# Kernel tuning notes

Measured on AMD Instinct MI355X. Metric: run time of the kernel, lower is better.

The kernel has to match this reference:

```python
import jax, jax.numpy as jnp
import numpy as np

TOKENS = 4096
IN_FEATURES = 4096
OUT_FEATURES = 4096
NNZ = 512  # nonzeros per output row, multiple of 4 so vectorize-pad is a no-op


def setup_inputs() -> dict:
    key = jax.random.key(0)
    k1, k2, k3, k4 = jax.random.split(key, 4)
    x = jax.random.normal(k1, (TOKENS, IN_FEATURES), dtype=jnp.float32)
    w = jax.random.normal(k2, (OUT_FEATURES, NNZ), dtype=jnp.float32)
    # sorted per-row column indices, mimicking nonzero() order of a pruned row
    mask = jnp.sort(
        jax.random.randint(k3, (OUT_FEATURES, NNZ), 0, IN_FEATURES, dtype=jnp.int32),
        axis=-1,
    )
    b = jax.random.normal(k4, (OUT_FEATURES,), dtype=jnp.float32)
    return {"input": x, "condensed_weight": w, "input_mask": mask, "bias": b}


def reference(input, condensed_weight, input_mask, bias):
    # y[t, o] = sum_k input[t, input_mask[o, k]] * condensed_weight[o, k] + bias[o]
    # Scatter condensed rows back to a dense [O, In] weight, then GEMM.
    # .add handles duplicate / padded (index 0, weight 0) entries exactly like
    # the gather-multiply-reduce formulation.
    O, K = condensed_weight.shape
    In = input.shape[-1]
    rows = jnp.arange(O, dtype=input_mask.dtype)[:, None]  # [O, 1]
    W = jnp.zeros((O, In), dtype=condensed_weight.dtype).at[rows, input_mask].add(condensed_weight)
    return input @ W.T + bias
```

## Files before the change

### kernel.cpp

```cpp
#include <hip/hip_runtime.h>
#include <hip/hip_bf16.h>
#include <stdint.h>

#define TOKENS 4096
#define IN_F   4096
#define OUT_F  4096
#define NNZ    512

using floatx4 = __attribute__((ext_vector_type(4))) float;
using bf16x8  = __attribute__((ext_vector_type(8))) __bf16;

__device__ __forceinline__ unsigned short f2bf(float f) {
    unsigned int u = __float_as_uint(f);
    u += 0x7FFFu + ((u >> 16) & 1u);
    return (unsigned short)(u >> 16);
}

__global__ __launch_bounds__(256) void prep_fused(
        const float* __restrict__ x,
        const float* __restrict__ w,
        const int*   __restrict__ mask,
        unsigned short* __restrict__ Xb,
        unsigned short* __restrict__ Wb) {
    __shared__ unsigned short row[IN_F];
    const int b = blockIdx.x;
    const int t = threadIdx.x;

    if (b < OUT_F) {
        uint4* rv = (uint4*)row;
        rv[t]       = make_uint4(0u, 0u, 0u, 0u);
        rv[t + 256] = make_uint4(0u, 0u, 0u, 0u);
        __syncthreads();

        const int base = b * NNZ;
#pragma unroll
        for (int e = 0; e < 2; ++e) {
            const int k = t + e * 256;
            const int idx = mask[base + k];
            if (k == 0 || mask[base + k - 1] != idx) {
                float s = w[base + k];
                int j = k + 1;
                while (j < NNZ && mask[base + j] == idx) { s += w[base + j]; ++j; }
                row[idx] = f2bf(s);
            }
        }
        __syncthreads();

        uint4* out = (uint4*)(Wb + (size_t)b * IN_F);
        out[t]       = rv[t];
        out[t + 256] = rv[t + 256];
    } else {
        const int i = (b - OUT_F) * 256 + t;
        const float4* xv = (const float4*)x;
        float4 a = xv[2 * i];
        float4 c = xv[2 * i + 1];
        uint4 o;
        o.x = (unsigned)f2bf(a.x) | ((unsigned)f2bf(a.y) << 16);
        o.y = (unsigned)f2bf(a.z) | ((unsigned)f2bf(a.w) << 16);
        o.z = (unsigned)f2bf(c.x) | ((unsigned)f2bf(c.y) << 16);
        o.w = (unsigned)f2bf(c.z) | ((unsigned)f2bf(c.w) << 16);
        ((uint4*)Xb)[i] = o;
    }
}


#define GLL16(src, dst) \
    __builtin_amdgcn_global_load_lds((__attribute__((address_space(1))) void*)(src), \
                                     (__attribute__((address_space(3))) void*)(dst), 16, 0, 0)

__global__ __launch_bounds__(512, 2) void gemm_bt_bias(
        const unsigned short* __restrict__ A,
        const unsigned short* __restrict__ B,
        const float* __restrict__ bias,
        float* __restrict__ C) {
    __shared__ unsigned short As[2][16384];
    __shared__ unsigned short Bs[2][16384];

    const int tid  = threadIdx.x;
    const int wave = tid >> 6;
    const int lane = tid & 63;
    const int lq   = lane >> 4;
    const int lm   = lane & 15;
    const int lm7  = lm & 7;
    const int wm2  = wave >> 2;
    const int wn4  = wave & 3;

    const int bid = blockIdx.x;
    const int swz = (bid & 7) * 32 + (bid >> 3);
    const int m0  = (swz >> 4) << 8;
    const int n0  = (swz & 15) << 8;

    const int r   = tid >> 3;
    const int cse = ((tid & 7) ^ (r & 7)) * 8;
    const int oAX0 = (m0 + r)       * IN_F + cse;
    const int oAX1 = (m0 + 128 + r) * IN_F + cse;
    const int oAY0 = (m0 +  64 + r) * IN_F + cse;
    const int oAY1 = (m0 + 192 + r) * IN_F + cse;
    const int bc_  = (r >> 5) * 64 + (r & 31);
    const int oBU0 = (n0 + bc_)        * IN_F + cse;
    const int oBU1 = (n0 + 128 + bc_)  * IN_F + cse;
    const int oBV0 = (n0 +  32 + bc_)  * IN_F + cse;
    const int oBV1 = (n0 + 160 + bc_)  * IN_F + cse;
    const int wofs = wave * 512;

#define STAGE_AX(bb, kk) { GLL16(A + oAX0 + (kk), &As[bb][        wofs]); \
                           GLL16(A + oAX1 + (kk), &As[bb][ 4096 + wofs]); }
#define STAGE_AY(bb, kk) { GLL16(A + oAY0 + (kk), &As[bb][ 8192 + wofs]); \
                           GLL16(A + oAY1 + (kk), &As[bb][12288 + wofs]); }
#define STAGE_BU(bb, kk) { GLL16(B + oBU0 + (kk), &Bs[bb][        wofs]); \
                           GLL16(B + oBU1 + (kk), &Bs[bb][ 4096 + wofs]); }
#define STAGE_BV(bb, kk) { GLL16(B + oBV0 + (kk), &Bs[bb][ 8192 + wofs]); \
                           GLL16(B + oBV1 + (kk), &Bs[bb][12288 + wofs]); }

    const int ck0 = (lq ^ lm7) * 8;
    const int ck1 = ck0 ^ 32;
    const int aX  = (wm2 * 64 + lm) * 64;
    const int aY  = aX + 8192;
    const int bU  = (wn4 * 32 + lm) * 64;
    const int bV  = bU + 8192;

    floatx4 acc[8][4] = {};
    bf16x8 af[4][2], bu[2][2], bv[2][2];

    STAGE_AX(0, 0); STAGE_BU(0, 0); STAGE_BV(0, 0); STAGE_AY(0, 0);
    STAGE_AX(1, 64); STAGE_BU(1, 64); STAGE_BV(1, 64);
    asm volatile("s_waitcnt vmcnt(6)" ::: "memory");
    __builtin_amdgcn_s_barrier();

#define TILE_STEP(T, BB)                                                          \
    {                                                                             \
        const unsigned short* sA = As[BB];                                        \
        const unsigned short* sB = Bs[BB];                                        \
        const int kk1 = ((T) + 1 < 64 ? (T) + 1 : 63) * 64;                       \
        const int kk2 = ((T) + 2 < 64 ? (T) + 2 : 63) * 64;                       \
                                                      \
        _Pragma("unroll")                                                         \
        for (int mi = 0; mi < 4; ++mi) {                                          \
            af[mi][0] = *(const bf16x8*)(sA + aX + mi * 1024 + ck0);              \
            af[mi][1] = *(const bf16x8*)(sA + aX + mi * 1024 + ck1);              \
        }                                                                         \
        _Pragma("unroll")                                                         \
        for (int ni = 0; ni < 2; ++ni) {                                          \
            bu[ni][0] = *(const bf16x8*)(sB + bU + ni * 1024 + ck0);              \
            bu[ni][1] = *(const bf16x8*)(sB + bU + ni * 1024 + ck1);              \
        }                                                                         \
        STAGE_AY((BB) ^ 1, kk1);                                                  \
        asm volatile("s_waitcnt lgkmcnt(8)" ::: "memory");                        \
        __builtin_amdgcn_s_barrier();                                             \
        asm volatile("s_waitcnt lgkmcnt(0)" ::: "memory");                        \
        __builtin_amdgcn_s_setprio(1);                                            \
        _Pragma("unroll")                                                         \
        for (int mi = 0; mi < 4; ++mi)                                            \
            _Pragma("unroll")                                                     \
            for (int ni = 0; ni < 2; ++ni) {                                      \
                acc[mi][ni] = __builtin_amdgcn_mfma_f32_16x16x32_bf16(            \
                    af[mi][0], bu[ni][0], acc[mi][ni], 0, 0, 0);                  \
                acc[mi][ni] = __builtin_amdgcn_mfma_f32_16x16x32_bf16(            \
                    af[mi][1], bu[ni][1], acc[mi][ni], 0, 0, 0);                  \
            }                                                                     \
        __builtin_amdgcn_s_setprio(0);                                            \
        __builtin_amdgcn_s_barrier();                                             \
                                                      \
        _Pragma("unroll")                                                         \
        for (int ni = 0; ni < 2; ++ni) {                                          \
            bv[ni][0] = *(const bf16x8*)(sB + bV + ni * 1024 + ck0);              \
            bv[ni][1] = *(const bf16x8*)(sB + bV + ni * 1024 + ck1);              \
        }                                                                         \
        STAGE_AX((BB), kk2);                                                      \
        __builtin_amdgcn_s_barrier();                                             \
        asm volatile("s_waitcnt lgkmcnt(0)" ::: "memory");                        \
        __builtin_amdgcn_s_setprio(1);                                            \
        _Pragma("unroll")                                                         \
        for (int mi = 0; mi < 4; ++mi)                                            \
            _Pragma("unroll")                                                     \
            for (int ni = 0; ni < 2; ++ni) {                                      \
                acc[mi][2 + ni] = __builtin_amdgcn_mfma_f32_16x16x32_bf16(        \
                    af[mi][0], bv[ni][0], acc[mi][2 + ni], 0, 0, 0);              \
                acc[mi][2 + ni] = __builtin_amdgcn_mfma_f32_16x16x32_bf16(        \
                    af[mi][1], bv[ni][1], acc[mi][2 + ni], 0, 0, 0);              \
            }                                                                     \
        __builtin_amdgcn_s_setprio(0);                                            \
        __builtin_amdgcn_s_barrier();                                             \
                                                      \
        _Pragma("unroll")                                                         \
        for (int mi = 0; mi < 4; ++mi) {                                          \
            af[mi][0] = *(const bf16x8*)(sA + aY + mi * 1024 + ck0);              \
            af[mi][1] = *(const bf16x8*)(sA + aY + mi * 1024 + ck1);              \
        }                                                                         \
        STAGE_BU((BB), kk2);                                                      \
        __builtin_amdgcn_s_barrier();                                             \
        asm volatile("s_waitcnt lgkmcnt(0)" ::: "memory");                        \
        __builtin_amdgcn_s_setprio(1);                                            \
        _Pragma("unroll")                                                         \
        for (int mi = 0; mi < 4; ++mi)                                            \
            _Pragma("unroll")                                                     \
            for (int ni = 0; ni < 2; ++ni) {                                      \
                acc[4 + mi][2 + ni] = __builtin_amdgcn_mfma_f32_16x16x32_bf16(    \
                    af[mi][0], bv[ni][0], acc[4 + mi][2 + ni], 0, 0, 0);          \
                acc[4 + mi][2 + ni] = __builtin_amdgcn_mfma_f32_16x16x32_bf16(    \
                    af[mi][1], bv[ni][1], acc[4 + mi][2 + ni], 0, 0, 0);          \
            }                                                                     \
        __builtin_amdgcn_s_setprio(0);                                            \
        __builtin_amdgcn_s_barrier();                                             \
                                \
        STAGE_BV((BB), kk2);                                                      \
        __builtin_amdgcn_s_barrier();                                             \
        __builtin_amdgcn_s_setprio(1);                                            \
        _Pragma("unroll")                                                         \
        for (int mi = 0; mi < 4; ++mi)                                            \
            _Pragma("unroll")                                                     \
            for (int ni = 0; ni < 2; ++ni) {                                      \
                acc[4 + mi][ni] = __builtin_amdgcn_mfma_f32_16x16x32_bf16(        \
                    af[mi][0], bu[ni][0], acc[4 + mi][ni], 0, 0, 0);              \
                acc[4 + mi][ni] = __builtin_amdgcn_mfma_f32_16x16x32_bf16(        \
                    af[mi][1], bu[ni][1], acc[4 + mi][ni], 0, 0, 0);              \
            }                                                                     \
        __builtin_amdgcn_s_setprio(0);                                            \
        asm volatile("s_waitcnt vmcnt(6)" ::: "memory");                          \
        __builtin_amdgcn_s_barrier();                                             \
    }

    for (int tt = 0; tt < 32; ++tt) {
        TILE_STEP(2 * tt,     0);
        TILE_STEP(2 * tt + 1, 1);
    }

#pragma unroll
    for (int ni = 0; ni < 4; ++ni) {
        const int n = n0 + wn4 * 64 + ni * 16 + lm;
        const float bb = bias[n];
#pragma unroll
        for (int mi = 0; mi < 8; ++mi) {
            const int mb = m0 + wm2 * 128 + mi * 16 + lq * 4;
#pragma unroll
            for (int rr = 0; rr < 4; ++rr) {
                C[(size_t)(mb + rr) * OUT_F + n] = acc[mi][ni][rr] + bb;
            }
        }
    }
}

extern "C" void kernel_launch(void* const* d_in, const int* in_sizes, int n_in,
                              void* d_out, int out_size, void* d_ws, size_t ws_size,
                              hipStream_t stream) {
    const float* x    = (const float*)d_in[0];
    const float* w    = (const float*)d_in[1];
    const int*   mask = (const int*)d_in[2];
    const float* bias = (const float*)d_in[3];
    float* out = (float*)d_out;

    unsigned short* Xb = (unsigned short*)d_ws;
    unsigned short* Wb = Xb + (size_t)TOKENS * IN_F;

    prep_fused<<<OUT_F + 8192, 256, 0, stream>>>(x, w, mask, Xb, Wb);
    gemm_bt_bias<<<dim3(256), dim3(512), 0, stream>>>(Xb, Wb, bias, out);
}
```

Before: 253.8 us.

## Restructure prep kernel to wave-per-row densify and multi-element cast, nontemporal output stores

The weight densify step now assigns one wavefront per output row, with four rows per block, and uses vectorized int4/float4 loads plus a per-lane run-merge. This removes block-wide barriers and the per-element scan over neighbouring mask entries. The input cast blocks each process four chunks, so the grid shrinks from 12288 to 3072 blocks. The GEMM epilogue writes C with nontemporal stores to avoid polluting cache. Fewer blocks could reduce the latency hiding available in the prep kernel.

```diff
diff --git a/kernel.cpp b/kernel.cpp
--- a/kernel.cpp
+++ b/kernel.cpp
@@ -22,44 +22,65 @@
         const int*   __restrict__ mask,
         unsigned short* __restrict__ Xb,
         unsigned short* __restrict__ Wb) {
-    __shared__ unsigned short row[IN_F];
+    __shared__ unsigned short rows[4][IN_F];
     const int b = blockIdx.x;
     const int t = threadIdx.x;
 
-    if (b < OUT_F) {
+    if (b < 1024) {
+        const int wave = t >> 6;
+        const int lane = t & 63;
+        const int rrow = b * 4 + wave;
+        unsigned short* row = rows[wave];
         uint4* rv = (uint4*)row;
-        rv[t]       = make_uint4(0u, 0u, 0u, 0u);
-        rv[t + 256] = make_uint4(0u, 0u, 0u, 0u);
-        __syncthreads();
-
-        const int base = b * NNZ;
-#pragma unroll
-        for (int e = 0; e < 2; ++e) {
-            const int k = t + e * 256;
-            const int idx = mask[base + k];
-            if (k == 0 || mask[base + k - 1] != idx) {
-                float s = w[base + k];
-                int j = k + 1;
-                while (j < NNZ && mask[base + j] == idx) { s += w[base + j]; ++j; }
-                row[idx] = f2bf(s);
+        const uint4 z = make_uint4(0u, 0u, 0u, 0u);
+#pragma unroll
+        for (int j = 0; j < 8; ++j) rv[lane + 64 * j] = z;
+
+        const int base = rrow * NNZ;
+        const int4*   m4 = (const int4*)(mask + base);
+        const float4* w4 = (const float4*)(w + base);
+        const int4   ma = m4[2 * lane], mb2 = m4[2 * lane + 1];
+        const float4 wa = w4[2 * lane], wb2 = w4[2 * lane + 1];
+        const int   mk[8] = {ma.x, ma.y, ma.z, ma.w, mb2.x, mb2.y, mb2.z, mb2.w};
+        const float wk[8] = {wa.x, wa.y, wa.z, wa.w, wb2.x, wb2.y, wb2.z, wb2.w};
+
+        int   cur = (lane == 0) ? -1 : mask[base + 8 * lane - 1];
+        float s   = 0.0f;
+        bool  own = false;
+#pragma unroll
+        for (int e = 0; e < 8; ++e) {
+            if (mk[e] != cur) {
+                if (own) row[cur] = f2bf(s);
+                cur = mk[e]; s = wk[e]; own = true;
+            } else if (own) {
+                s += wk[e];
             }
         }
-        __syncthreads();
-
-        uint4* out = (uint4*)(Wb + (size_t)b * IN_F);
-        out[t]       = rv[t];
-        out[t + 256] = rv[t + 256];
+        if (own) {
+            int g = 8 * lane + 8;
+            while (g < NNZ && mask[base + g] == cur) { s += w[base + g]; ++g; }
+            row[cur] = f2bf(s);
+        }
+
+        uint4* out = (uint4*)(Wb + (size_t)rrow * IN_F);
+#pragma unroll
+        for (int j = 0; j < 8; ++j) out[lane + 64 * j] = rv[lane + 64 * j];
     } else {
-        const int i = (b - OUT_F) * 256 + t;
+        const int b1 = b - 1024;
         const float4* xv = (const float4*)x;
-        float4 a = xv[2 * i];
-        float4 c = xv[2 * i + 1];
-        uint4 o;
-        o.x = (unsigned)f2bf(a.x) | ((unsigned)f2bf(a.y) << 16);
-        o.y = (unsigned)f2bf(a.z) | ((unsigned)f2bf(a.w) << 16);
-        o.z = (unsigned)f2bf(c.x) | ((unsigned)f2bf(c.y) << 16);
-        o.w = (unsigned)f2bf(c.z) | ((unsigned)f2bf(c.w) << 16);
-        ((uint4*)Xb)[i] = o;
+        uint4* xo = (uint4*)Xb;
+#pragma unroll
+        for (int it = 0; it < 4; ++it) {
+            const int i = b1 * 256 + t + it * 524288;
+            float4 a = xv[2 * i];
+            float4 c = xv[2 * i + 1];
+            uint4 o;
+            o.x = (unsigned)f2bf(a.x) | ((unsigned)f2bf(a.y) << 16);
+            o.y = (unsigned)f2bf(a.z) | ((unsigned)f2bf(a.w) << 16);
+            o.z = (unsigned)f2bf(c.x) | ((unsigned)f2bf(c.y) << 16);
+            o.w = (unsigned)f2bf(c.z) | ((unsigned)f2bf(c.w) << 16);
+            xo[i] = o;
+        }
     }
 }
 
@@ -234,7 +255,8 @@
             const int mb = m0 + wm2 * 128 + mi * 16 + lq * 4;
 #pragma unroll
             for (int rr = 0; rr < 4; ++rr) {
-                C[(size_t)(mb + rr) * OUT_F + n] = acc[mi][ni][rr] + bb;
+                __builtin_nontemporal_store(acc[mi][ni][rr] + bb,
+                                            &C[(size_t)(mb + rr) * OUT_F + n]);
             }
         }
     }
@@ -252,6 +274,6 @@
     unsigned short* Xb = (unsigned short*)d_ws;
     unsigned short* Wb = Xb + (size_t)TOKENS * IN_F;
 
-    prep_fused<<<OUT_F + 8192, 256, 0, stream>>>(x, w, mask, Xb, Wb);
+    prep_fused<<<3072, 256, 0, stream>>>(x, w, mask, Xb, Wb);
     gemm_bt_bias<<<dim3(256), dim3(512), 0, stream>>>(Xb, Wb, bias, out);
 }
```

Result: no change. 254.8 us (+0.4%).
